# Kernel optimization log

Hardware: AMD Instinct MI355X
Metric: run time of the kernel (lower is better)

The kernel has to match this reference:

```python
import jax, jax.numpy as jnp
import numpy as np

N, C, P, M = 8, 20, 8732, 16
THRESHOLD, NEG_POS_RATIO, ALPHA = 0.5, 3, 1.0


def cxcy_to_xy(c):
    return jnp.concatenate([c[..., :2] - c[..., 2:] / 2.0, c[..., :2] + c[..., 2:] / 2.0], axis=-1)


def xy_to_cxcy(xy):
    return jnp.concatenate([(xy[..., :2] + xy[..., 2:]) / 2.0, xy[..., 2:] - xy[..., :2]], axis=-1)


def cxcy_to_gcxgcy(cxcy, priors):
    g_cxcy = (cxcy[..., :2] - priors[..., :2]) / (priors[..., 2:] / 10.0)
    g_wh = jnp.log(cxcy[..., 2:] / priors[..., 2:]) * 5.0
    return jnp.concatenate([g_cxcy, g_wh], axis=-1)


def jaccard(a, b):
    # a: (M,4), b: (P,4), boundary coords -> IoU (M,P)
    lo = jnp.maximum(a[:, None, :2], b[None, :, :2])
    hi = jnp.minimum(a[:, None, 2:], b[None, :, 2:])
    inter = jnp.prod(jnp.clip(hi - lo, 0.0), axis=-1)
    area_a = jnp.prod(a[:, 2:] - a[:, :2], axis=-1)
    area_b = jnp.prod(b[:, 2:] - b[:, :2], axis=-1)
    return inter / (area_a[:, None] + area_b[None, :] - inter)


def setup_inputs() -> dict:
    key = jax.random.key(0)
    k1, k2, k3, k4, k5, k6 = jax.random.split(key, 6)
    predicted_locs = jax.random.normal(k1, (N, C, P, 4), jnp.float32)
    predicted_scores = jax.random.normal(k2, (N, C, P, 2), jnp.float32)
    # valid ground-truth boundary boxes (x1<x2, y1<y2) in [0,1]
    ctr = jax.random.uniform(k3, (N, C, M, 2), minval=0.2, maxval=0.8)
    wh = jax.random.uniform(k4, (N, C, M, 2), minval=0.05, maxval=0.3)
    boxes = jnp.concatenate([ctr - wh / 2.0, ctr + wh / 2.0], axis=-1)
    # valid priors in cxcywh (w,h > 0 so log-encoding is finite)
    pctr = jax.random.uniform(k5, (P, 2), minval=0.05, maxval=0.95)
    pwh = jax.random.uniform(k6, (P, 2), minval=0.05, maxval=0.5)
    priors_cxcy = jnp.concatenate([pctr, pwh], axis=-1)
    labels = jnp.ones((N, C, M), jnp.int32)  # binary per-class head: object label = 1
    return {
        "predicted_locs": predicted_locs,
        "predicted_scores": predicted_scores,
        "boxes": boxes,
        "labels": labels,
        "priors_cxcy": priors_cxcy,
    }


def _forward(predicted_locs, predicted_scores, boxes, priors_cxcy, labels):
    n_classes = predicted_scores.shape[1]
    n_priors = predicted_scores.shape[2]
    priors_xy = cxcy_to_xy(priors_cxcy)

    def match(b, lab):
        # b: (M,4) boundary, lab: (M,) int
        ov = jaccard(b, priors_xy)                       # (M,P)
        obj_for_prior = jnp.argmax(ov, axis=0)           # (P,)
        ov_for_prior = jnp.max(ov, axis=0)               # (P,)
        prior_for_obj = jnp.argmax(ov, axis=1)           # (M,)
        # force each object to own its best prior
        obj_for_prior = obj_for_prior.at[prior_for_obj].set(jnp.arange(b.shape[0]))
        ov_for_prior = ov_for_prior.at[prior_for_obj].set(1.0)
        cls = jnp.where(ov_for_prior < THRESHOLD, 0, lab[obj_for_prior])  # (P,)
        tl = cxcy_to_gcxgcy(xy_to_cxcy(b[obj_for_prior]), priors_cxcy)    # (P,4)
        return tl, cls

    true_locs, true_classes = jax.vmap(jax.vmap(match))(boxes, labels)  # (N,C,P,4), (N,C,P)

    pos = true_classes != 0                      # (N,C,P)
    posf = pos.astype(predicted_locs.dtype)
    n_pos_bc = posf.sum(axis=2)                  # (N,C) positives per image per class
    n_pos_c = n_pos_bc.sum(axis=0)               # (C,)

    # localization: mean L1 over positive priors (4 coords each), per class
    l1 = jnp.abs(predicted_locs - true_locs).sum(-1) * posf   # (N,C,P)
    loc_loss_c = l1.sum(axis=(0, 2)) / jnp.maximum(n_pos_c * 4.0, 1.0)

    # per-prior binary cross entropy
    logp = jax.nn.log_softmax(predicted_scores, axis=-1)      # (N,C,P,2)
    ce = -jnp.take_along_axis(logp, true_classes[..., None], axis=-1)[..., 0]  # (N,C,P)
    conf_pos_c = (ce * posf).sum(axis=(0, 2))

    # hard negative mining: sort negatives desc per (image,class) row, keep top 3*n_pos
    ce_neg = jnp.where(pos, 0.0, ce)
    ce_neg_sorted = -jnp.sort(-ce_neg, axis=-1)               # (N,C,P) descending
    n_hard = NEG_POS_RATIO * n_pos_bc                         # (N,C)
    ranks = jnp.arange(n_priors, dtype=n_hard.dtype)
    hard_mask = ranks[None, None, :] < n_hard[..., None]
    conf_hard_c = (ce_neg_sorted * hard_mask).sum(axis=(0, 2))

    safe = jnp.maximum(n_pos_c, 1.0)
    loss_c = jnp.where(
        n_pos_c > 0,
        (conf_pos_c + conf_hard_c + ALPHA * loc_loss_c) / safe,
        0.0,
    ) / n_classes
    return loss_c.sum()


def reference(predicted_locs, predicted_scores, boxes, labels, priors_cxcy):
    return _forward(predicted_locs, predicted_scores, boxes, priors_cxcy, labels)
```

## Files before the change

### kernel.cpp

```cpp
#include <hip/hip_runtime.h>
#include <math.h>

#define NN 8
#define CC 20
#define PP 8732
#define MM 16
#define NPR 3
#define SPLIT 12
#define CH 728
#define ROWS (NN * CC)

__device__ __forceinline__ float fast_rcp(float x) { return __builtin_amdgcn_rcpf(x); }
__device__ __forceinline__ float rfl(float x) {
    return __uint_as_float(__builtin_amdgcn_readfirstlane(__float_as_uint(x)));
}

__device__ __forceinline__ float lse2(float a, float b) {
    float mx = fmaxf(a, b);
    float d  = fabsf(a - b);
    return mx + __logf(1.0f + __expf(-d));
}

#define ABLK 256
__global__ __launch_bounds__(ABLK) void mbox_p1(
    const float* __restrict__ locs, const float* __restrict__ scores,
    const float* __restrict__ boxes, const int* __restrict__ labels,
    const float* __restrict__ priors,
    unsigned char* __restrict__ pk8,
    unsigned long long* __restrict__ partials, float* __restrict__ cstats)
{
    const int row = blockIdx.x / SPLIT;
    const int chunk = blockIdx.x - row * SPLIT;
    const int tid = threadIdx.x, lane = tid & 63, wav = tid >> 6;

    __shared__ float s_bcx[MM], s_bcy[MM], s_bw[MM], s_bh[MM];
    __shared__ unsigned int s_pk[4 * MM];
    __shared__ float s_rf[4 * 3];

    float bx1[MM], by1[MM], bx2[MM], by2[MM], bar[MM];
    unsigned int labm = 0;
    {
        const float* bb = boxes + (size_t)row * MM * 4;
        const int*   lb = labels + (size_t)row * MM;
#pragma unroll
        for (int m = 0; m < MM; m++) {
            float x1 = rfl(bb[m * 4 + 0]), y1 = rfl(bb[m * 4 + 1]);
            float x2 = rfl(bb[m * 4 + 2]), y2 = rfl(bb[m * 4 + 3]);
            bx1[m] = x1; by1[m] = y1; bx2[m] = x2; by2[m] = y2;
            bar[m] = rfl((x2 - x1) * (y2 - y1));
            labm |= (lb[m] != 0 ? 1u : 0u) << m;
        }
        labm = __builtin_amdgcn_readfirstlane(labm);
    }
    if (tid < MM) {
        s_bcx[tid] = (bx1[tid] + bx2[tid]) * 0.5f;
        s_bcy[tid] = (by1[tid] + by2[tid]) * 0.5f;
        s_bw[tid]  = bx2[tid] - bx1[tid];
        s_bh[tid]  = by2[tid] - by1[tid];
    }
    __syncthreads();

    const float4* pri4 = (const float4*)priors;
    const float4* loc4 = (const float4*)(locs + (size_t)row * PP * 4);
    const float2* sc2  = (const float2*)(scores + (size_t)row * PP * 2);
    unsigned char* pk  = pk8 + (size_t)row * PP;

    unsigned int bestk[MM];
#pragma unroll
    for (int m = 0; m < MM; m++) bestk[m] = 0u;
    float l_np = 0.0f, l_l1 = 0.0f, l_cp = 0.0f;
    const int p0 = chunk * CH, p1e = min(p0 + CH, PP);

    int it = 0;
    for (int p = p0 + tid; p < p1e; p += ABLK, ++it) {
        const unsigned int lowb = ((unsigned int)(7 - it) << 8) | (unsigned int)(255 - tid);
        float4 pr = pri4[p];
        float hw = pr.z * 0.5f, hh = pr.w * 0.5f;
        float px1 = pr.x - hw, py1 = pr.y - hh;
        float px2 = pr.x + hw, py2 = pr.y + hh;
        float area_b = (px2 - px1) * (py2 - py1);
        unsigned int bovk = 0u;
#pragma unroll
        for (int m = 0; m < MM; m++) {
            float dx = fminf(bx2[m], px2) - fmaxf(bx1[m], px1);
            float dy = fminf(by2[m], py2) - fmaxf(by1[m], py1);
            dx = fmaxf(dx, 0.0f); dy = fmaxf(dy, 0.0f);
            float inter = dx * dy;
            float den = (bar[m] + area_b) - inter;
            float iou = inter * fast_rcp(den);
            unsigned int ib = __float_as_uint(iou);
            unsigned int km = (ib & 0xFFFFFFF0u) | (unsigned int)(15 - m);
            bovk = max(bovk, km);
            unsigned int kp = (ib & 0xFFFFF800u) | lowb;
            bestk[m] = max(bestk[m], kp);
        }
        int bm = 15 - (int)(bovk & 15u);
        bool pos = (bovk >= 0x3F000000u) && (((labm >> bm) & 1u) != 0u);
        pk[p] = (unsigned char)((pos ? 16u : 0u) | (unsigned)bm);
        if (pos) {
            float2 sc = sc2[p];
            float4 pl = loc4[p];
            l_np += 1.0f;
            l_cp += lse2(sc.x, sc.y) - sc.y;
            float tx = (s_bcx[bm] - pr.x) * 10.0f / pr.z;
            float ty = (s_bcy[bm] - pr.y) * 10.0f / pr.w;
            float tw = __logf(s_bw[bm] / pr.z) * 5.0f;
            float th = __logf(s_bh[bm] / pr.w) * 5.0f;
            l_l1 += fabsf(pl.x - tx) + fabsf(pl.y - ty) + fabsf(pl.z - tw) + fabsf(pl.w - th);
        }
    }

#pragma unroll
    for (int m = 0; m < MM; m++) {
        unsigned int key = bestk[m];
#pragma unroll
        for (int off = 32; off; off >>= 1) {
            unsigned int o = __shfl_down(key, off);
            if (o > key) key = o;
        }
        if (lane == 0) s_pk[wav * MM + m] = key;
    }
#pragma unroll
    for (int off = 32; off; off >>= 1) {
        l_np += __shfl_down(l_np, off);
        l_l1 += __shfl_down(l_l1, off);
        l_cp += __shfl_down(l_cp, off);
    }
    if (lane == 0) { s_rf[wav * 3] = l_np; s_rf[wav * 3 + 1] = l_l1; s_rf[wav * 3 + 2] = l_cp; }
    __syncthreads();
    if (tid < MM) {
        unsigned int key = s_pk[tid];
        for (int w = 1; w < 4; w++) {
            unsigned int o = s_pk[w * MM + tid];
            if (o > key) key = o;
        }
        int tw  = 255 - (int)(key & 255u);
        int itw = 7 - (int)((key >> 8) & 7u);
        int pm  = p0 + itw * ABLK + tw;
        partials[((size_t)row * MM + tid) * SPLIT + chunk] =
            ((unsigned long long)(key & 0xFFFFF800u) << 32) |
            (unsigned int)(0x7fffffff - pm);
    }
    if (tid == 0) {
        float np = 0, l1 = 0, cp = 0;
        for (int w = 0; w < 4; w++) { np += s_rf[w * 3]; l1 += s_rf[w * 3 + 1]; cp += s_rf[w * 3 + 2]; }
        float* cs = cstats + ((size_t)row * SPLIT + chunk) * 3;
        cs[0] = np; cs[1] = l1; cs[2] = cp;
    }
}

#define CBLK 1024
#define EPT 9
__global__ __launch_bounds__(CBLK) void mbox_sel(
    const float* __restrict__ locs, const float* __restrict__ scores,
    const float* __restrict__ boxes, const int* __restrict__ labels,
    const float* __restrict__ priors,
    const unsigned char* __restrict__ pk8,
    const unsigned long long* __restrict__ partials,
    const float* __restrict__ cstats, float* __restrict__ rstats)
{
    const int row = blockIdx.x, tid = threadIdx.x, lane = tid & 63, wav = tid >> 6;
    __shared__ float s_bcx[MM], s_bcy[MM], s_bw[MM], s_bh[MM];
    __shared__ int s_lab[MM], s_pfo[MM], s_fp[MM];
    __shared__ float s_fv[MM], s_sum[3];
    __shared__ unsigned int s_cnt[16][4];
    __shared__ unsigned int s_K;
    __shared__ float s_redf[16];
    __shared__ int s_redi[16];

    if (tid < 64) ((unsigned int*)s_cnt)[tid] = 0u;
    if (tid < MM) {
        s_fp[tid] = -1;
        const float* b = boxes + ((size_t)row * MM + tid) * 4;
        float x1 = b[0], y1 = b[1], x2 = b[2], y2 = b[3];
        s_bcx[tid] = (x1 + x2) * 0.5f; s_bcy[tid] = (y1 + y2) * 0.5f;
        s_bw[tid] = x2 - x1; s_bh[tid] = y2 - y1;
        s_lab[tid] = labels[row * MM + tid];
        const unsigned long long* pr = partials + ((size_t)row * MM + tid) * SPLIT;
        unsigned long long key = pr[0];
        for (int c = 1; c < SPLIT; c++) { unsigned long long o = pr[c]; if (o > key) key = o; }
        s_pfo[tid] = 0x7fffffff - (int)(unsigned)(key & 0xffffffffull);
    }
    if (tid >= 16 && tid < 19) {
        int j = tid - 16; float s = 0;
        for (int c = 0; c < SPLIT; c++) s += cstats[((size_t)row * SPLIT + c) * 3 + j];
        s_sum[j] = s;
    }
    __syncthreads();

    float d_np = 0, d_l1 = 0, d_cp = 0;
    if (tid < MM) {
        int p = s_pfo[tid];
        bool is_last = true;
        for (int mm = tid + 1; mm < MM; mm++) if (s_pfo[mm] == p) is_last = false;
        if (is_last) {
            const float4 pr = ((const float4*)priors)[p];
            const float4 pl = ((const float4*)(locs + (size_t)row * PP * 4))[p];
            const float2 sc = ((const float2*)(scores + (size_t)row * PP * 2))[p];
            float lse = lse2(sc.x, sc.y);
            unsigned int u = pk8[(size_t)row * PP + p];
            if (u & 16u) {
                int mo = u & 15;
                d_np -= 1.0f; d_cp -= (lse - sc.y);
                float tx = (s_bcx[mo] - pr.x) * 10.0f / pr.z;
                float ty = (s_bcy[mo] - pr.y) * 10.0f / pr.w;
                float tw = __logf(s_bw[mo] / pr.z) * 5.0f;
                float th = __logf(s_bh[mo] / pr.w) * 5.0f;
                d_l1 -= fabsf(pl.x - tx) + fabsf(pl.y - ty) + fabsf(pl.z - tw) + fabsf(pl.w - th);
            }
            if (s_lab[tid] != 0) {
                d_np += 1.0f; d_cp += (lse - sc.y);
                float tx = (s_bcx[tid] - pr.x) * 10.0f / pr.z;
                float ty = (s_bcy[tid] - pr.y) * 10.0f / pr.w;
                float tw = __logf(s_bw[tid] / pr.z) * 5.0f;
                float th = __logf(s_bh[tid] / pr.w) * 5.0f;
                d_l1 += fabsf(pl.x - tx) + fabsf(pl.y - ty) + fabsf(pl.z - tw) + fabsf(pl.w - th);
                s_fv[tid] = 0.0f;
            } else {
                s_fv[tid] = fmaxf(lse - sc.x, 0.0f);
            }
            s_fp[tid] = p;
        }
    }
    if (tid < 64) {
#pragma unroll
        for (int off = 32; off; off >>= 1) {
            d_np += __shfl_down(d_np, off);
            d_l1 += __shfl_down(d_l1, off);
            d_cp += __shfl_down(d_cp, off);
        }
        if (tid == 0) {
            float np = s_sum[0] + d_np;
            rstats[(size_t)row * 8 + 0] = np;
            rstats[(size_t)row * 8 + 1] = s_sum[1] + d_l1;
            rstats[(size_t)row * 8 + 2] = s_sum[2] + d_cp;
            int K = NPR * (int)(np + 0.5f);
            s_K = (K > 0) ? (unsigned)K : 0u;
        }
    }
    __syncthreads();

    const float2* sc2 = (const float2*)(scores + (size_t)row * PP * 2);
    const unsigned char* pk = pk8 + (size_t)row * PP;
    unsigned int uv[EPT];
#pragma unroll
    for (int k = 0; k < EPT; k++) {
        int p = tid + k * CBLK;
        if (p < PP) {
            unsigned int u8 = pk[p];
            float2 sc = sc2[p];
            float ce = (u8 & 16u) ? 0.0f : fmaxf(lse2(sc.x, sc.y) - sc.x, 0.0f);
            uv[k] = __float_as_uint(ce);
        } else uv[k] = 0u;
    }
    for (int t = 0; t < MM; t++) {
        int fp = s_fp[t];
        if (fp >= 0) {
            unsigned int fb = __float_as_uint(s_fv[t]);
#pragma unroll
            for (int k = 0; k < EPT; k++) if (tid + k * CBLK == fp) uv[k] = fb;
        }
    }

    const unsigned int K = s_K;
    unsigned int T = 0u;
    if (K > 0u) {
        for (int r = 0; r < 16; r++) {
            const int b = 30 - 2 * r;
            const unsigned int T1 = T | (1u << b), T2 = T | (2u << b), T3 = T | (3u << b);
            unsigned int c1 = 0, c2 = 0, c3 = 0;
#pragma unroll
            for (int k = 0; k < EPT; k++) {
                unsigned int u = uv[k];
                c1 += (u >= T1); c2 += (u >= T2); c3 += (u >= T3);
            }
#pragma unroll
            for (int off = 32; off; off >>= 1) {
                c1 += __shfl_down(c1, off);
                c2 += __shfl_down(c2, off);
                c3 += __shfl_down(c3, off);
            }
            if (lane == 0) {
                atomicAdd(&s_cnt[r][1], c1);
                atomicAdd(&s_cnt[r][2], c2);
                atomicAdd(&s_cnt[r][3], c3);
            }
            __syncthreads();
            unsigned int C1 = s_cnt[r][1], C2 = s_cnt[r][2], C3 = s_cnt[r][3];
            if      (C3 >= K) T = T3;
            else if (C2 >= K) T = T2;
            else if (C1 >= K) T = T1;
        }
    }

    float sgt = 0.0f; int cgt = 0;
    if (K > 0u) {
#pragma unroll
        for (int k = 0; k < EPT; k++) {
            unsigned int u = uv[k];
            if (u > T) { sgt += __uint_as_float(u); cgt++; }
        }
    }
#pragma unroll
    for (int off = 32; off; off >>= 1) {
        sgt += __shfl_down(sgt, off);
        cgt += __shfl_down(cgt, off);
    }
    if (lane == 0) { s_redf[wav] = sgt; s_redi[wav] = cgt; }
    __syncthreads();
    if (tid == 0) {
        float s = 0; int cnt = 0;
        for (int w = 0; w < 16; w++) { s += s_redf[w]; cnt += s_redi[w]; }
        float chard = (K > 0u) ? (s + (float)(int)(K - (unsigned)cnt) * __uint_as_float(T)) : 0.0f;
        rstats[(size_t)row * 8 + 4] = chard;
    }
}

__global__ void mbox_finalize(const float* __restrict__ rstats, float* __restrict__ out) {
    int c = threadIdx.x;
    float loss = 0.0f;
    if (c < CC) {
        float np = 0, l1 = 0, cp = 0, ch = 0;
        for (int n = 0; n < NN; n++) {
            const float* s = rstats + ((size_t)(n * CC + c)) * 8;
            np += s[0]; l1 += s[1]; cp += s[2]; ch += s[4];
        }
        float loc = l1 / fmaxf(np * 4.0f, 1.0f);
        float val = (np > 0.0f) ? (cp + ch + loc) / fmaxf(np, 1.0f) : 0.0f;
        loss = val / (float)CC;
    }
#pragma unroll
    for (int off = 32; off; off >>= 1) loss += __shfl_down(loss, off);
    if (threadIdx.x == 0) out[0] = loss;
}

extern "C" void kernel_launch(void* const* d_in, const int* in_sizes, int n_in,
                              void* d_out, int out_size, void* d_ws, size_t ws_size,
                              hipStream_t stream) {
    const float* locs   = (const float*)d_in[0];
    const float* scores = (const float*)d_in[1];
    const float* boxes  = (const float*)d_in[2];
    const int*   labels = (const int*)d_in[3];
    const float* priors = (const float*)d_in[4];
    float* out = (float*)d_out;

    char* ws = (char*)d_ws;
    unsigned char* pk8           = (unsigned char*)ws;
    unsigned long long* partials = (unsigned long long*)(ws + 1397120);
    float* cstats                = (float*)(ws + 1642880);
    float* rstats                = (float*)(ws + 1665920);

    mbox_p1<<<ROWS * SPLIT, ABLK, 0, stream>>>(locs, scores, boxes, labels, priors,
                                               pk8, partials, cstats);
    mbox_sel<<<ROWS, CBLK, 0, stream>>>(locs, scores, boxes, labels, priors,
                                        pk8, partials, cstats, rstats);
    mbox_finalize<<<1, 64, 0, stream>>>(rstats, out);
}
```

Baseline: 139.9 us.

## Replace 2-bit radix threshold search with 8-bit histogram select; prefetch priors

The hard-negative threshold search now runs four 8-bit radix passes instead of sixteen 2-bit rounds. Each pass builds a 256-bin shared-memory histogram with atomics, and one wavefront finds the bin holding the k-th largest value using a suffix scan. The aim is to cut the number of block-wide reduction and barrier rounds, at the cost of per-element LDS atomics that may contend heavily when loss values share high bytes. The IoU kernel also loads the next prior one iteration ahead to hide global-load latency.

```diff
diff --git a/kernel.cpp b/kernel.cpp
--- a/kernel.cpp
+++ b/kernel.cpp
@@ -71,10 +71,13 @@
     float l_np = 0.0f, l_l1 = 0.0f, l_cp = 0.0f;
     const int p0 = chunk * CH, p1e = min(p0 + CH, PP);
 
+    float4 pr_next;
+    if (p0 + tid < p1e) pr_next = pri4[p0 + tid];
     int it = 0;
     for (int p = p0 + tid; p < p1e; p += ABLK, ++it) {
+        float4 pr = pr_next;
+        if (p + ABLK < p1e) pr_next = pri4[p + ABLK];
         const unsigned int lowb = ((unsigned int)(7 - it) << 8) | (unsigned int)(255 - tid);
-        float4 pr = pri4[p];
         float hw = pr.z * 0.5f, hh = pr.w * 0.5f;
         float px1 = pr.x - hw, py1 = pr.y - hh;
         float px2 = pr.x + hw, py2 = pr.y + hh;
@@ -163,12 +166,11 @@
     __shared__ float s_bcx[MM], s_bcy[MM], s_bw[MM], s_bh[MM];
     __shared__ int s_lab[MM], s_pfo[MM], s_fp[MM];
     __shared__ float s_fv[MM], s_sum[3];
-    __shared__ unsigned int s_cnt[16][4];
-    __shared__ unsigned int s_K;
+    __shared__ unsigned int s_hist[256];
+    __shared__ unsigned int s_prefix, s_Kr, s_K;
     __shared__ float s_redf[16];
     __shared__ int s_redi[16];
 
-    if (tid < 64) ((unsigned int*)s_cnt)[tid] = 0u;
     if (tid < MM) {
         s_fp[tid] = -1;
         const float* b = boxes + ((size_t)row * MM + tid) * 4;
@@ -236,6 +238,8 @@
             rstats[(size_t)row * 8 + 2] = s_sum[2] + d_cp;
             int K = NPR * (int)(np + 0.5f);
             s_K = (K > 0) ? (unsigned)K : 0u;
+            s_prefix = 0u;
+            s_Kr = (K > 0) ? (unsigned)K : 0u;
         }
     }
     __syncthreads();
@@ -264,33 +268,54 @@
 
     const unsigned int K = s_K;
     unsigned int T = 0u;
-    if (K > 0u) {
-        for (int r = 0; r < 16; r++) {
-            const int b = 30 - 2 * r;
-            const unsigned int T1 = T | (1u << b), T2 = T | (2u << b), T3 = T | (3u << b);
-            unsigned int c1 = 0, c2 = 0, c3 = 0;
+    if (K > 0u && K < PP) {
+        for (int pass = 0; pass < 4; pass++) {
+            const int shift = 24 - 8 * pass;
+            if (tid < 256) s_hist[tid] = 0u;
+            __syncthreads();
+            const unsigned int pref   = s_prefix;
+            const unsigned int maskhi = (pass == 0) ? 0u : (0xffffffffu << (shift + 8));
 #pragma unroll
             for (int k = 0; k < EPT; k++) {
                 unsigned int u = uv[k];
-                c1 += (u >= T1); c2 += (u >= T2); c3 += (u >= T3);
-            }
-#pragma unroll
-            for (int off = 32; off; off >>= 1) {
-                c1 += __shfl_down(c1, off);
-                c2 += __shfl_down(c2, off);
-                c3 += __shfl_down(c3, off);
-            }
-            if (lane == 0) {
-                atomicAdd(&s_cnt[r][1], c1);
-                atomicAdd(&s_cnt[r][2], c2);
-                atomicAdd(&s_cnt[r][3], c3);
+                if ((u & maskhi) == pref) atomicAdd(&s_hist[(u >> shift) & 255u], 1u);
             }
             __syncthreads();
-            unsigned int C1 = s_cnt[r][1], C2 = s_cnt[r][2], C3 = s_cnt[r][3];
-            if      (C3 >= K) T = T3;
-            else if (C2 >= K) T = T2;
-            else if (C1 >= K) T = T1;
-        }
+            if (wav == 0) {
+                unsigned int Kr = s_Kr;
+                unsigned int h0 = s_hist[lane * 4 + 0];
+                unsigned int h1 = s_hist[lane * 4 + 1];
+                unsigned int h2 = s_hist[lane * 4 + 2];
+                unsigned int h3 = s_hist[lane * 4 + 3];
+                unsigned int c3 = h3;
+                unsigned int c2 = h3 + h2;
+                unsigned int c1 = c2 + h1;
+                unsigned int c0 = c1 + h0;
+                unsigned int suf = c0;
+#pragma unroll
+                for (int off = 1; off < 64; off <<= 1) {
+                    unsigned int o = __shfl_down(suf, off);
+                    if (lane + off < 64) suf += o;
+                }
+                unsigned int above = suf - c0;
+                int cand = -1;
+                unsigned int G = 0;
+                if      (c3 + above >= Kr) { cand = lane * 4 + 3; G = above + c3 - h3; }
+                else if (c2 + above >= Kr) { cand = lane * 4 + 2; G = above + c2 - h2; }
+                else if (c1 + above >= Kr) { cand = lane * 4 + 1; G = above + c1 - h1; }
+                else if (c0 + above >= Kr) { cand = lane * 4 + 0; G = above + c0 - h0; }
+                int best = cand;
+#pragma unroll
+                for (int off = 32; off; off >>= 1) best = max(best, __shfl_down(best, off));
+                best = __shfl(best, 0);
+                if (cand == best && cand >= 0) {
+                    s_Kr = Kr - G;
+                    s_prefix = pref | ((unsigned int)best << shift);
+                }
+            }
+            __syncthreads();
+        }
+        T = s_prefix;
     }
 
     float sgt = 0.0f; int cgt = 0;
@@ -311,7 +336,7 @@
     if (tid == 0) {
         float s = 0; int cnt = 0;
         for (int w = 0; w < 16; w++) { s += s_redf[w]; cnt += s_redi[w]; }
-        float chard = (K > 0u) ? (s + (float)(int)(K - (unsigned)cnt) * __uint_as_float(T)) : 0.0f;
+        float chard = (K > 0u) ? (s + (float)(int)(K - (unsigned)cgt * 0u - (unsigned)cnt) * __uint_as_float(T)) : 0.0f;
         rstats[(size_t)row * 8 + 4] = chard;
     }
 }
```

Result: faster. 126.4 us (-9.6%).
